# Optimization experiments

Hardware: AMD Instinct MI355X
Metric: run time of the kernel (lower is better)

The kernel has to match this reference:

```python
import jax, jax.numpy as jnp
import numpy as np

BATCH, SEQ, IN, HID, OUT = 4096, 512, 2, 128, 1


def setup_inputs() -> dict:
    key = jax.random.key(0)
    k_x, k_wih, k_bih, k_who, k_bho = jax.random.split(key, 5)
    s = 1.0 / np.sqrt(IN + HID)
    return {
        "x": jax.random.normal(k_x, (BATCH, SEQ, IN), dtype=jnp.float32),
        "W_ih": jax.random.normal(k_wih, (HID, IN + HID), dtype=jnp.float32) * s,
        "b_ih": jax.random.normal(k_bih, (HID,), dtype=jnp.float32) * s,
        "W_ho": jax.random.normal(k_who, (OUT, HID), dtype=jnp.float32) / np.sqrt(HID),
        "b_bho" if False else "b_ho": jax.random.normal(k_bho, (OUT,), dtype=jnp.float32) / np.sqrt(HID),
    }


def reference(x, W_ih, b_ih, W_ho, b_ho):
    # x: [B, T, I]. Elman cell: h = tanh([x_t, h] @ W_ih^T + b_ih)
    B = x.shape[0]
    h0 = jnp.zeros((B, W_ih.shape[0]), dtype=x.dtype)
    # split W_ih into input and hidden blocks (equivalent to concat+matmul)
    W_x = W_ih[:, : x.shape[-1]]   # [H, I]
    W_h = W_ih[:, x.shape[-1] :]   # [H, H]

    def step(h, x_t):
        h_new = jnp.tanh(x_t @ W_x.T + h @ W_h.T + b_ih)
        return h_new, None

    xs = jnp.swapaxes(x, 0, 1)  # [T, B, I] for scan over time
    h_final, _ = jax.lax.scan(step, h0, xs)
    return h_final @ W_ho.T + b_ho  # [B, OUT]
```

## Files before the change

kernel.cpp:

```cpp
#include <hip/hip_runtime.h>


constexpr int BATCH   = 4096;
constexpr int SEQ     = 512;
constexpr int INP     = 2;
constexpr int HID     = 128;
constexpr int BM      = 16;
constexpr int THREADS = 512;
constexpr int XCHUNK  = 128;

typedef short bf16x8 __attribute__((ext_vector_type(8)));
typedef float f32x4  __attribute__((ext_vector_type(4)));

__device__ inline unsigned short f2bf(float f) {
    unsigned u = __float_as_uint(f);
    return (unsigned short)((u + 0x7FFFu + ((u >> 16) & 1u)) >> 16);
}
__device__ inline float bf2f(unsigned short s) {
    return __uint_as_float(((unsigned)s) << 16);
}
__device__ inline unsigned cvt_pk_bf16(float a, float b) {
    unsigned r;
    asm("v_cvt_pk_bf16_f32 %0, %1, %2" : "=v"(r) : "v"(a), "v"(b));
    return r;
}

__global__ __launch_bounds__(THREADS, 2)
void elman_mfma10(const float* __restrict__ x,
                  const float* __restrict__ W_ih,
                  const float* __restrict__ b_ih,
                  const float* __restrict__ W_ho,
                  const float* __restrict__ b_ho,
                  float* __restrict__ out)
{
    __shared__ unsigned short hlds[2][2][BM][HID];
    __shared__ float2 xs[XCHUNK][BM];
    __shared__ float red[BM][8];

    const int tid  = threadIdx.x;
    const int lane = tid & 63;
    const int w    = tid >> 6;
    const int l15  = lane & 15;
    const int g    = lane >> 4;
    const int B0   = blockIdx.x * BM;

    bf16x8 whi[4], wlo[4];
    {
        const float* Wrow = W_ih + (size_t)(w * 16 + l15) * (INP + HID) + INP;
        #pragma unroll
        for (int kt = 0; kt < 4; ++kt) {
            const int k0 = kt * 32 + g * 8;
            #pragma unroll
            for (int i = 0; i < 8; ++i) {
                const float wv = Wrow[k0 + i];
                const unsigned short hi = f2bf(wv);
                whi[kt][i] = (short)hi;
                wlo[kt][i] = (short)f2bf(wv - bf2f(hi));
            }
        }
    }

    float wx0v[4], wx1v[4], bjv[4], whov[4];
    #pragma unroll
    for (int reg = 0; reg < 4; ++reg) {
        const int jj = w * 16 + g * 4 + reg;
        const float* Wr = W_ih + (size_t)jj * (INP + HID);
        wx0v[reg] = Wr[0];
        wx1v[reg] = Wr[1];
        bjv[reg]  = b_ih[jj];
        whov[reg] = W_ho[jj];
    }

    int roff[4];
    #pragma unroll
    for (int kt = 0; kt < 4; ++kt)
        roff[kt] = l15 * 256 + ((kt * 64 + g * 16) ^ (l15 << 4));
    const int woff = l15 * 256 + (((w * 32 + (g & 2) * 8)) ^ (l15 << 4)) + (g & 1) * 8;

    reinterpret_cast<float4*>(hlds)[tid]       = float4{0.f, 0.f, 0.f, 0.f};
    reinterpret_cast<float4*>(hlds)[tid + 512] = float4{0.f, 0.f, 0.f, 0.f};

    const int sr = tid >> 5;
    const int so = (tid & 31) * 8;
    {
        const float* src = x + (size_t)(B0 + sr) * (SEQ * INP) + so;
        const float4 v0 = *reinterpret_cast<const float4*>(src);
        const float4 v1 = *reinterpret_cast<const float4*>(src + 4);
        const int t0 = so >> 1;
        xs[t0 + 0][sr] = float2{v0.x, v0.y};
        xs[t0 + 1][sr] = float2{v0.z, v0.w};
        xs[t0 + 2][sr] = float2{v1.x, v1.y};
        xs[t0 + 3][sr] = float2{v1.z, v1.w};
    }
    __syncthreads();

    char* hbA = (char*)&hlds[0][0][0][0];
    char* lbA = (char*)&hlds[0][1][0][0];
    char* hbB = (char*)&hlds[1][0][0][0];
    char* lbB = (char*)&hlds[1][1][0][0];

    float hv[4] = {0.f, 0.f, 0.f, 0.f};

#define RNN_STEP(HP, LP, HN, LN, TT)                                           \
    {                                                                          \
        bf16x8 ahi[4], alo[4];                                                 \
        _Pragma("unroll")                                                      \
        for (int kt = 0; kt < 4; ++kt) {                                       \
            ahi[kt] = *reinterpret_cast<const bf16x8*>((HP) + roff[kt]);       \
            alo[kt] = *reinterpret_cast<const bf16x8*>((LP) + roff[kt]);       \
        }                                                                      \
        f32x4 a0 = {0.f, 0.f, 0.f, 0.f};                                       \
        f32x4 a1 = {0.f, 0.f, 0.f, 0.f};                                       \
        f32x4 a2 = {0.f, 0.f, 0.f, 0.f};                                       \
        _Pragma("unroll")                                                      \
        for (int kt = 0; kt < 4; ++kt) {                                       \
            a0 = __builtin_amdgcn_mfma_f32_16x16x32_bf16(whi[kt], ahi[kt], a0, 0, 0, 0); \
            a1 = __builtin_amdgcn_mfma_f32_16x16x32_bf16(whi[kt], alo[kt], a1, 0, 0, 0); \
            a2 = __builtin_amdgcn_mfma_f32_16x16x32_bf16(wlo[kt], ahi[kt], a2, 0, 0, 0); \
        }                                                                      \
        const float2 xv = xs[(TT)][l15];                                       \
        float hcur[4];                                                         \
        _Pragma("unroll")                                                      \
        for (int reg = 0; reg < 4; ++reg) {                                    \
            const float acc = (a0[reg] + a1[reg] + a2[reg])                    \
                            + fmaf(wx0v[reg], xv.x, fmaf(wx1v[reg], xv.y, bjv[reg])); \
            const float e = __expf(acc + acc);                                 \
            hcur[reg] = 1.0f - __fdividef(2.0f, e + 1.0f);      \
            hv[reg]   = hcur[reg];                                             \
        }                                                                      \
        const unsigned c01 = cvt_pk_bf16(hcur[0], hcur[1]);                    \
        const unsigned c23 = cvt_pk_bf16(hcur[2], hcur[3]);                    \
        const float h0b = __uint_as_float(c01 << 16);                          \
        const float h1b = __uint_as_float(c01 & 0xFFFF0000u);                  \
        const float h2b = __uint_as_float(c23 << 16);                          \
        const float h3b = __uint_as_float(c23 & 0xFFFF0000u);                  \
        const unsigned l01 = cvt_pk_bf16(hcur[0] - h0b, hcur[1] - h1b);        \
        const unsigned l23 = cvt_pk_bf16(hcur[2] - h2b, hcur[3] - h3b);        \
        *reinterpret_cast<uint2*>((HN) + woff) = uint2{c01, c23};              \
        *reinterpret_cast<uint2*>((LN) + woff) = uint2{l01, l23};              \
        __syncthreads();                                                       \
    }

    #pragma unroll 1
    for (int t2 = 0; t2 < SEQ; t2 += 2) {
        const int tt = t2 & (XCHUNK - 1);
        if (t2 && tt == 0) {
            const float* src = x + (size_t)(B0 + sr) * (SEQ * INP)
                                 + (size_t)(t2 >> 7) * (XCHUNK * INP) + so;
            const float4 v0 = *reinterpret_cast<const float4*>(src);
            const float4 v1 = *reinterpret_cast<const float4*>(src + 4);
            const int t0 = so >> 1;
            xs[t0 + 0][sr] = float2{v0.x, v0.y};
            xs[t0 + 1][sr] = float2{v0.z, v0.w};
            xs[t0 + 2][sr] = float2{v1.x, v1.y};
            xs[t0 + 3][sr] = float2{v1.z, v1.w};
            __syncthreads();
        }
        RNN_STEP(hbA, lbA, hbB, lbB, tt)
        RNN_STEP(hbB, lbB, hbA, lbA, tt + 1)
    }
#undef RNN_STEP

    float part = 0.f;
    #pragma unroll
    for (int reg = 0; reg < 4; ++reg) part = fmaf(whov[reg], hv[reg], part);
    part += __shfl_xor(part, 16);
    part += __shfl_xor(part, 32);
    if (lane < 16) red[l15][w] = part;
    __syncthreads();
    if (tid < BM) {
        float s = b_ho[0];
        #pragma unroll
        for (int q = 0; q < 8; ++q) s += red[tid][q];
        out[B0 + tid] = s;
    }
}

extern "C" void kernel_launch(void* const* d_in, const int* in_sizes, int n_in,
                              void* d_out, int out_size, void* d_ws, size_t ws_size,
                              hipStream_t stream)
{
    (void)in_sizes; (void)n_in; (void)out_size; (void)d_ws; (void)ws_size;
    const float* x    = (const float*)d_in[0];
    const float* W_ih = (const float*)d_in[1];
    const float* b_ih = (const float*)d_in[2];
    const float* W_ho = (const float*)d_in[3];
    const float* b_ho = (const float*)d_in[4];
    float* out = (float*)d_out;

    dim3 grid(BATCH / BM);
    dim3 block(THREADS);
    elman_mfma10<<<grid, block, 0, stream>>>(x, W_ih, b_ih, W_ho, b_ho, out);
}
```

Before: 312.6 us.

## Prefetch x directly into registers and use LDS-only barrier per step

Removes the LDS staging buffer for x and its periodic chunk reloads. Each lane now prefetches the next two timesteps' inputs from global memory into registers one iteration ahead. The per-step __syncthreads is replaced with an inline asm barrier that waits only on lgkmcnt (LDS) rather than on all outstanding memory. This keeps the in-flight global prefetch from stalling the step barrier and drops the extra sync at chunk boundaries. The risks are that the global load latency now sits in every step's critical path, and that correctness depends on the hand-written waitcnt.

New measurement: 302.5 us. 3.2% less time.

```diff
diff --git a/kernel.cpp b/kernel.cpp
--- a/kernel.cpp
+++ b/kernel.cpp
@@ -7,7 +7,6 @@
 constexpr int HID     = 128;
 constexpr int BM      = 16;
 constexpr int THREADS = 512;
-constexpr int XCHUNK  = 128;
 
 typedef short bf16x8 __attribute__((ext_vector_type(8)));
 typedef float f32x4  __attribute__((ext_vector_type(4)));
@@ -24,9 +23,12 @@
     asm("v_cvt_pk_bf16_f32 %0, %1, %2" : "=v"(r) : "v"(a), "v"(b));
     return r;
 }
+__device__ inline void lds_barrier() {
+    asm volatile("s_waitcnt lgkmcnt(0)\n\ts_barrier" ::: "memory");
+}
 
 __global__ __launch_bounds__(THREADS, 2)
-void elman_mfma10(const float* __restrict__ x,
+void elman_mfma11(const float* __restrict__ x,
                   const float* __restrict__ W_ih,
                   const float* __restrict__ b_ih,
                   const float* __restrict__ W_ho,
@@ -34,7 +36,6 @@
                   float* __restrict__ out)
 {
     __shared__ unsigned short hlds[2][2][BM][HID];
-    __shared__ float2 xs[XCHUNK][BM];
     __shared__ float red[BM][8];
 
     const int tid  = threadIdx.x;
@@ -80,18 +81,10 @@
     reinterpret_cast<float4*>(hlds)[tid]       = float4{0.f, 0.f, 0.f, 0.f};
     reinterpret_cast<float4*>(hlds)[tid + 512] = float4{0.f, 0.f, 0.f, 0.f};
 
-    const int sr = tid >> 5;
-    const int so = (tid & 31) * 8;
-    {
-        const float* src = x + (size_t)(B0 + sr) * (SEQ * INP) + so;
-        const float4 v0 = *reinterpret_cast<const float4*>(src);
-        const float4 v1 = *reinterpret_cast<const float4*>(src + 4);
-        const int t0 = so >> 1;
-        xs[t0 + 0][sr] = float2{v0.x, v0.y};
-        xs[t0 + 1][sr] = float2{v0.z, v0.w};
-        xs[t0 + 2][sr] = float2{v1.x, v1.y};
-        xs[t0 + 3][sr] = float2{v1.z, v1.w};
-    }
+    const float* xrow = x + (size_t)(B0 + l15) * (SEQ * INP);
+    float2 xv0 = *reinterpret_cast<const float2*>(xrow);
+    float2 xv1 = *reinterpret_cast<const float2*>(xrow + INP);
+
     __syncthreads();
 
     char* hbA = (char*)&hlds[0][0][0][0];
@@ -101,7 +94,7 @@
 
     float hv[4] = {0.f, 0.f, 0.f, 0.f};
 
-#define RNN_STEP(HP, LP, HN, LN, TT)                                           \
+#define RNN_STEP(HP, LP, HN, LN, XV)                                           \
     {                                                                          \
         bf16x8 ahi[4], alo[4];                                                 \
         _Pragma("unroll")                                                      \
@@ -118,7 +111,7 @@
             a1 = __builtin_amdgcn_mfma_f32_16x16x32_bf16(whi[kt], alo[kt], a1, 0, 0, 0); \
             a2 = __builtin_amdgcn_mfma_f32_16x16x32_bf16(wlo[kt], ahi[kt], a2, 0, 0, 0); \
         }                                                                      \
-        const float2 xv = xs[(TT)][l15];                                       \
+        const float2 xv = (XV);                                                \
         float hcur[4];                                                         \
         _Pragma("unroll")                                                      \
         for (int reg = 0; reg < 4; ++reg) {                                    \
@@ -138,26 +131,20 @@
         const unsigned l23 = cvt_pk_bf16(hcur[2] - h2b, hcur[3] - h3b);        \
         *reinterpret_cast<uint2*>((HN) + woff) = uint2{c01, c23};              \
         *reinterpret_cast<uint2*>((LN) + woff) = uint2{l01, l23};              \
-        __syncthreads();                                                       \
+        lds_barrier();                                                         \
     }
 
     #pragma unroll 1
     for (int t2 = 0; t2 < SEQ; t2 += 2) {
-        const int tt = t2 & (XCHUNK - 1);
-        if (t2 && tt == 0) {
-            const float* src = x + (size_t)(B0 + sr) * (SEQ * INP)
-                                 + (size_t)(t2 >> 7) * (XCHUNK * INP) + so;
-            const float4 v0 = *reinterpret_cast<const float4*>(src);
-            const float4 v1 = *reinterpret_cast<const float4*>(src + 4);
-            const int t0 = so >> 1;
-            xs[t0 + 0][sr] = float2{v0.x, v0.y};
-            xs[t0 + 1][sr] = float2{v0.z, v0.w};
-            xs[t0 + 2][sr] = float2{v1.x, v1.y};
-            xs[t0 + 3][sr] = float2{v1.z, v1.w};
-            __syncthreads();
-        }
-        RNN_STEP(hbA, lbA, hbB, lbB, tt)
-        RNN_STEP(hbB, lbB, hbA, lbA, tt + 1)
+        const int tn = (t2 + 2 < SEQ) ? (t2 + 2) : 0;
+        const float2 xn0 = *reinterpret_cast<const float2*>(xrow + (size_t)tn * INP);
+        const float2 xn1 = *reinterpret_cast<const float2*>(xrow + (size_t)tn * INP + INP);
+
+        RNN_STEP(hbA, lbA, hbB, lbB, xv0)
+        RNN_STEP(hbB, lbB, hbA, lbA, xv1)
+
+        xv0 = xn0;
+        xv1 = xn1;
     }
 #undef RNN_STEP
 
@@ -190,5 +177,5 @@
 
     dim3 grid(BATCH / BM);
     dim3 block(THREADS);
-    elman_mfma10<<<grid, block, 0, stream>>>(x, W_ih, b_ih, W_ho, b_ho, out);
+    elman_mfma11<<<grid, block, 0, stream>>>(x, W_ih, b_ih, W_ho, b_ho, out);
 }
```
